# Kernel optimization log

Measured on AMD Instinct MI355X. Metric: run time of the kernel, lower is better.

## Reference

```python
import jax, jax.numpy as jnp
import numpy as np

N = 50000      # nodes
E = 800000     # edges
IN = 128       # in_channels
HID = 64       # hidden_channels (out per head)
H = 4          # heads
ED = 64        # edge_dim
HC = H * HID   # concat output width


def segment_softmax(logits, seg, num_segments):
    # logits: [E, H], softmax over edges sharing the same destination node
    m = jax.ops.segment_max(logits, seg, num_segments=num_segments)
    m = jnp.where(jnp.isfinite(m), m, 0.0)
    e = jnp.exp(logits - m[seg])
    s = jax.ops.segment_sum(e, seg, num_segments=num_segments)
    return e / (s[seg] + 1e-16)


def gatv2_layer(x, src, dst, edge_attr, Wl, bl, Wr, br, We, att, bias):
    # GATv2Conv (PyG, concat=True, negative_slope=0.2), dropout off (eval)
    Hh, C = att.shape
    xl = (x @ Wl + bl).reshape(-1, Hh, C)   # [N,H,C] source transform
    xr = (x @ Wr + br).reshape(-1, Hh, C)   # [N,H,C] target transform
    ee = (edge_attr @ We).reshape(-1, Hh, C)  # [E,H,C]
    m = jax.nn.leaky_relu(xl[src] + xr[dst] + ee, 0.2)  # [E,H,C]
    logits = jnp.einsum('ehc,hc->eh', m, att)           # [E,H]
    alpha = segment_softmax(logits, dst, x.shape[0])    # [E,H]
    out = jax.ops.segment_sum(alpha[:, :, None] * xl[src], dst,
                              num_segments=x.shape[0])  # [N,H,C]
    return out.reshape(x.shape[0], Hh * C) + bias


def setup_inputs() -> dict:
    key = jax.random.key(0)
    ks = jax.random.split(key, 20)
    g = lambda k, shape, s=0.05: (jax.random.normal(k, shape, jnp.float32) * s)
    inp = {
        'x': jax.random.normal(ks[0], (N, IN), jnp.float32),
        'edge_index': jax.random.randint(ks[1], (2, E), 0, N, dtype=jnp.int32),
        'edge_attr': jax.random.normal(ks[2], (E, ED), jnp.float32),
        # layer 1: in_channels -> heads*hidden
        'Wl1': g(ks[3], (IN, HC)), 'bl1': jnp.zeros((HC,), jnp.float32),
        'Wr1': g(ks[4], (IN, HC)), 'br1': jnp.zeros((HC,), jnp.float32),
        'We1': g(ks[5], (ED, HC)),
        'att1': g(ks[6], (H, HID)), 'bias1': jnp.zeros((HC,), jnp.float32),
        # layer 2: heads*hidden -> heads*hidden
        'Wl2': g(ks[7], (HC, HC)), 'bl2': jnp.zeros((HC,), jnp.float32),
        'Wr2': g(ks[8], (HC, HC)), 'br2': jnp.zeros((HC,), jnp.float32),
        'We2': g(ks[9], (ED, HC)),
        'att2': g(ks[10], (H, HID)), 'bias2': jnp.zeros((HC,), jnp.float32),
    }
    return inp


def reference(x, edge_index, edge_attr,
              Wl1, bl1, Wr1, br1, We1, att1, bias1,
              Wl2, bl2, Wr2, br2, We2, att2, bias2):
    src, dst = edge_index[0], edge_index[1]
    h1 = gatv2_layer(x, src, dst, edge_attr, Wl1, bl1, Wr1, br1, We1, att1, bias1)
    h2 = gatv2_layer(h1, src, dst, edge_attr, Wl2, bl2, Wr2, br2, We2, att2, bias2)
    return h2
```

## Files before the change

kernel.cpp:

```cpp
#include <hip/hip_runtime.h>
#include <math.h>

#define NN 50000
#define NE 800000

#define LRELU(v) fmaxf((v), 0.2f * (v))

typedef __attribute__((ext_vector_type(4))) float f32x4;
typedef __attribute__((ext_vector_type(8))) short bf16x8;

static __device__ __forceinline__ unsigned short f2bf(float f) {
  union { float f; unsigned int i; } c; c.f = f;
  unsigned int r = c.i + 0x7fff + ((c.i >> 16) & 1);
  return (unsigned short)(r >> 16);
}
static __device__ __forceinline__ float bflo(unsigned int u) {
  union { unsigned int i; float f; } c; c.i = u << 16; return c.f;
}
static __device__ __forceinline__ float bfhi(unsigned int u) {
  union { unsigned int i; float f; } c; c.i = u & 0xffff0000u; return c.f;
}

__global__ __launch_bounds__(256)
void conv_all(const float* __restrict__ We1, unsigned short* __restrict__ wef1,
              const float* __restrict__ We2, unsigned short* __restrict__ wef2,
              const float* __restrict__ Wl1, unsigned short* __restrict__ wlf1,
              const float* __restrict__ Wr1, unsigned short* __restrict__ wrf1,
              const float* __restrict__ Wl2, unsigned short* __restrict__ wlf2,
              const float* __restrict__ Wr2, unsigned short* __restrict__ wrf2) {
  const int y = blockIdx.y;
  const int g = blockIdx.x * 256 + threadIdx.x;
  if (y < 2) {
    if (g >= 16384) return;
    const float* We = y ? We2 : We1;
    unsigned short* wef = y ? wef2 : wef1;
    const int j = g & 7;
    const int l = (g >> 3) & 63;
    const int t = g >> 9;
    const int n = t & 15, half = t >> 4;
    const int k = half * 32 + (l >> 4) * 8 + j;
    const int c = ((l & 15) >> 2) * 64 + n * 4 + (l & 3);
    wef[g] = f2bf(We[(size_t)k * 256 + c]);
  } else {
    const int K = (y < 4) ? 128 : 256;
    if (g >= K * 256) return;
    const float* W = (y == 2) ? Wl1 : (y == 3) ? Wr1 : (y == 4) ? Wl2 : Wr2;
    unsigned short* wf = (y == 2) ? wlf1 : (y == 3) ? wrf1
                       : (y == 4) ? wlf2 : wrf2;
    const int j = g & 7;
    const int l = (g >> 3) & 63;
    const int fn = g >> 9;
    const int n = fn & 15, ks = fn >> 4;
    const int k = ks * 32 + (l >> 4) * 8 + j;
    const int c = n * 16 + (l & 15);
    wf[g] = f2bf(W[(size_t)k * 256 + c]);
  }
}

template <int KS, int BF>
__global__ __launch_bounds__(256)
void gemm_mfma4(const void* __restrict__ Av,
                const unsigned short* __restrict__ wf0,
                const float* __restrict__ b0, unsigned short* __restrict__ out0,
                const unsigned short* __restrict__ wf1,
                const float* __restrict__ b1, unsigned short* __restrict__ out1) {
  const int mat = blockIdx.y & 1;
  const int nh  = blockIdx.y >> 1;
  const unsigned short* wf = mat ? wf1 : wf0;
  const float* bias        = mat ? b1 : b0;
  unsigned short* outb     = mat ? out1 : out0;

  const int tid = threadIdx.x;
  const int w = tid >> 6, l = tid & 63;
  const int lid = l & 15, lg = l >> 4;
  const int row  = blockIdx.x * 64 + w * 16 + lid;
  const bool rowok = row < NN;
  const int rowv = rowok ? row : NN - 1;
  const int K = KS * 32;

  bf16x8 bfr[KS];
  if (BF) {
    const unsigned short* A = (const unsigned short*)Av;
    const unsigned short* ap = A + (size_t)rowv * K + lg * 8;
#pragma unroll
    for (int ks = 0; ks < KS; ++ks)
      bfr[ks] = *(const bf16x8*)(ap + ks * 32);
  } else {
    const float* A = (const float*)Av;
    const float* ap = A + (size_t)rowv * K + lg * 8;
#pragma unroll
    for (int ks = 0; ks < KS; ++ks) {
      const float4 v0 = *(const float4*)(ap + ks * 32);
      const float4 v1 = *(const float4*)(ap + ks * 32 + 4);
      bf16x8 b;
      b[0]=f2bf(v0.x); b[1]=f2bf(v0.y); b[2]=f2bf(v0.z); b[3]=f2bf(v0.w);
      b[4]=f2bf(v1.x); b[5]=f2bf(v1.y); b[6]=f2bf(v1.z); b[7]=f2bf(v1.w);
      bfr[ks] = b;
    }
  }

  f32x4 acc[8];
#pragma unroll
  for (int n8 = 0; n8 < 8; ++n8) acc[n8] = (f32x4){0.f, 0.f, 0.f, 0.f};

#pragma unroll
  for (int ks = 0; ks < KS; ++ks)
#pragma unroll
    for (int n8 = 0; n8 < 8; ++n8) {
      const int n = nh * 8 + n8;
      const bf16x8 a = *(const bf16x8*)(wf + ((size_t)(ks * 16 + n) * 64 + l) * 8);
      acc[n8] = __builtin_amdgcn_mfma_f32_16x16x32_bf16(a, bfr[ks], acc[n8], 0, 0, 0);
    }

  if (rowok) {
#pragma unroll
    for (int n8 = 0; n8 < 8; ++n8) {
      const int c0 = (nh * 8 + n8) * 16 + lg * 4;
      const float4 bv = *(const float4*)(bias + c0);
      ushort4 o;
      o.x = f2bf(acc[n8][0] + bv.x); o.y = f2bf(acc[n8][1] + bv.y);
      o.z = f2bf(acc[n8][2] + bv.z); o.w = f2bf(acc[n8][3] + bv.w);
      *(ushort4*)(outb + (size_t)row * 256 + c0) = o;
    }
  }
}

__global__ __launch_bounds__(256)
void dst_hist(const int* __restrict__ dst, int* __restrict__ cnt) {
  const int e = blockIdx.x * 256 + threadIdx.x;
  if (e < NE) atomicAdd(&cnt[dst[e]], 1);
}

__global__ __launch_bounds__(1024)
void scan_bsum(const int* __restrict__ cnt, int* __restrict__ bsum, int n) {
  __shared__ int wsum[16];
  const int tid = threadIdx.x;
  const int lane = tid & 63, wid = tid >> 6;
  const int i = blockIdx.x * 1024 + tid;
  int v = (i < n) ? cnt[i] : 0;
#pragma unroll
  for (int off = 32; off >= 1; off >>= 1) v += __shfl_xor(v, off);
  if (lane == 0) wsum[wid] = v;
  __syncthreads();
  if (tid == 0) {
    int s = 0;
#pragma unroll
    for (int k = 0; k < 16; ++k) s += wsum[k];
    bsum[blockIdx.x] = s;
  }
}

__global__ __launch_bounds__(64)
void scan_bsum_scan(int* __restrict__ bsum, int* __restrict__ row_start,
                    int nb, int n) {
  const int lane = threadIdx.x;
  const int v = (lane < nb) ? bsum[lane] : 0;
  int incl = v;
#pragma unroll
  for (int off = 1; off < 64; off <<= 1) {
    const int t = __shfl_up(incl, off);
    if (lane >= off) incl += t;
  }
  if (lane < nb) bsum[lane] = incl - v;
  if (lane == 63) row_start[n] = incl;
}

__global__ __launch_bounds__(1024)
void scan_apply(int* __restrict__ cnt, const int* __restrict__ bsum,
                int* __restrict__ row_start, int n) {
  __shared__ int wsum[16];
  __shared__ int woff[16];
  const int tid = threadIdx.x;
  const int lane = tid & 63, wid = tid >> 6;
  const int i = blockIdx.x * 1024 + tid;
  const int v = (i < n) ? cnt[i] : 0;
  int incl = v;
#pragma unroll
  for (int off = 1; off < 64; off <<= 1) {
    const int t = __shfl_up(incl, off);
    if (lane >= off) incl += t;
  }
  if (lane == 63) wsum[wid] = incl;
  __syncthreads();
  if (wid == 0) {
    const int s = (lane < 16) ? wsum[lane] : 0;
    int si = s;
#pragma unroll
    for (int off = 1; off < 16; off <<= 1) {
      const int t = __shfl_up(si, off);
      if (lane >= off) si += t;
    }
    if (lane < 16) woff[lane] = si - s;
  }
  __syncthreads();
  if (i < n) {
    const int excl = bsum[blockIdx.x] + woff[wid] + incl - v;
    row_start[i] = excl;
    cnt[i] = excl;
  }
}

__global__ __launch_bounds__(256)
void bucket_fill(const int* __restrict__ src, const int* __restrict__ dst,
                 int* __restrict__ cur, int* __restrict__ eid,
                 int* __restrict__ ssrc, int* __restrict__ sdst) {
  const int e = blockIdx.x * 256 + threadIdx.x;
  if (e < NE) {
    const int d = dst[e];
    const int p = atomicAdd(&cur[d], 1);
    eid[p] = e;
    ssrc[p] = src[e];
    sdst[p] = d;
  }
}

__global__ __launch_bounds__(256)
void conv_eab(const float* __restrict__ ea, const int* __restrict__ eid,
              unsigned short* __restrict__ eab) {
  const int g = blockIdx.x * 256 + threadIdx.x;
  const int p = g >> 4, c4 = (g & 15) * 4;
  const int e = eid[p];
  const float4 v = *(const float4*)(ea + (size_t)e * 64 + c4);
  ushort4 o;
  o.x = f2bf(v.x); o.y = f2bf(v.y); o.z = f2bf(v.z); o.w = f2bf(v.w);
  *(ushort4*)(eab + (size_t)p * 64 + c4) = o;
}

static __device__ __forceinline__ float edge_epilogue(
    const unsigned short* __restrict__ xlp,
    const unsigned short* __restrict__ xrp,
    const float* __restrict__ attp,
    const unsigned short* __restrict__ wef,
    bf16x8 f0, bf16x8 f1, int l) {
  float ph = 0.f;
#pragma unroll
  for (int nn = 0; nn < 8; ++nn) {
    const bf16x8 w00 = *(const bf16x8*)(wef + ((size_t)(0  + 2 * nn)     * 64 + l) * 8);
    const bf16x8 w01 = *(const bf16x8*)(wef + ((size_t)(16 + 2 * nn)     * 64 + l) * 8);
    const bf16x8 w10 = *(const bf16x8*)(wef + ((size_t)(0  + 2 * nn + 1) * 64 + l) * 8);
    const bf16x8 w11 = *(const bf16x8*)(wef + ((size_t)(16 + 2 * nn + 1) * 64 + l) * 8);

    f32x4 a0 = (f32x4){0.f,0.f,0.f,0.f}, a1 = (f32x4){0.f,0.f,0.f,0.f};
    a0 = __builtin_amdgcn_mfma_f32_16x16x32_bf16(w00, f0, a0, 0, 0, 0);
    a0 = __builtin_amdgcn_mfma_f32_16x16x32_bf16(w01, f1, a0, 0, 0, 0);
    a1 = __builtin_amdgcn_mfma_f32_16x16x32_bf16(w10, f0, a1, 0, 0, 0);
    a1 = __builtin_amdgcn_mfma_f32_16x16x32_bf16(w11, f1, a1, 0, 0, 0);

    const int c0 = nn * 8;
    const uint4 xu = *(const uint4*)(xlp + c0);
    const uint4 ru = *(const uint4*)(xrp + c0);
    const float4 at0 = *(const float4*)(attp + c0);
    const float4 at1 = *(const float4*)(attp + c0 + 4);
    float v;
    v = a0[0] + bflo(xu.x) + bflo(ru.x); v = LRELU(v); ph += v * at0.x;
    v = a0[1] + bfhi(xu.x) + bfhi(ru.x); v = LRELU(v); ph += v * at0.y;
    v = a0[2] + bflo(xu.y) + bflo(ru.y); v = LRELU(v); ph += v * at0.z;
    v = a0[3] + bfhi(xu.y) + bfhi(ru.y); v = LRELU(v); ph += v * at0.w;
    v = a1[0] + bflo(xu.z) + bflo(ru.z); v = LRELU(v); ph += v * at1.x;
    v = a1[1] + bfhi(xu.z) + bfhi(ru.z); v = LRELU(v); ph += v * at1.y;
    v = a1[2] + bflo(xu.w) + bflo(ru.w); v = LRELU(v); ph += v * at1.z;
    v = a1[3] + bfhi(xu.w) + bfhi(ru.w); v = LRELU(v); ph += v * at1.w;
  }
  return ph;
}

template <int EAB>
__global__ __launch_bounds__(128)
void edge_logits_swap(const float* __restrict__ ea,
                      const unsigned short* __restrict__ eab,
                      const unsigned short* __restrict__ wef,
                      const unsigned short* __restrict__ xlb,
                      const unsigned short* __restrict__ xrb,
                      const float* __restrict__ att,
                      const int* __restrict__ eid,
                      const int* __restrict__ ssrc, const int* __restrict__ sdst,
                      float* __restrict__ elog) {
  __shared__ unsigned short sxl[2][16 * 264];

  const int tid = threadIdx.x;
  const int w = tid >> 6, l = tid & 63;
  const int lid = l & 15, lg = l >> 4;
  const int base = (blockIdx.x * 2 + w) * 32;
  const int pA = base + lid;
  const int pB = base + 16 + lid;

  unsigned short* myxl = sxl[w];
  const int srow_r = l >> 5;
  const int unit   = l & 31;

  bf16x8 fA0, fA1;
  if (EAB) {
    fA0 = *(const bf16x8*)(eab + (size_t)pA * 64 + lg * 8);
    fA1 = *(const bf16x8*)(eab + (size_t)pA * 64 + 32 + lg * 8);
  } else {
    const int e = eid[pA];
    const float* ap = ea + (size_t)e * 64 + lg * 8;
    const float4 v00 = *(const float4*)(ap);
    const float4 v01 = *(const float4*)(ap + 4);
    const float4 v10 = *(const float4*)(ap + 32);
    const float4 v11 = *(const float4*)(ap + 36);
    fA0[0]=f2bf(v00.x); fA0[1]=f2bf(v00.y); fA0[2]=f2bf(v00.z); fA0[3]=f2bf(v00.w);
    fA0[4]=f2bf(v01.x); fA0[5]=f2bf(v01.y); fA0[6]=f2bf(v01.z); fA0[7]=f2bf(v01.w);
    fA1[0]=f2bf(v10.x); fA1[1]=f2bf(v10.y); fA1[2]=f2bf(v10.z); fA1[3]=f2bf(v10.w);
    fA1[4]=f2bf(v11.x); fA1[5]=f2bf(v11.y); fA1[6]=f2bf(v11.z); fA1[7]=f2bf(v11.w);
  }
  const int dA = sdst[pA];

  uint4 gA[8];
#pragma unroll
  for (int i = 0; i < 8; ++i) {
    const int row = i * 2 + srow_r;
    const int srow = ssrc[base + row];
    gA[i] = *(const uint4*)(xlb + (size_t)srow * 256 + unit * 8);
  }

  bf16x8 fB0, fB1;
  if (EAB) {
    fB0 = *(const bf16x8*)(eab + (size_t)pB * 64 + lg * 8);
    fB1 = *(const bf16x8*)(eab + (size_t)pB * 64 + 32 + lg * 8);
  } else {
    const int e = eid[pB];
    const float* ap = ea + (size_t)e * 64 + lg * 8;
    const float4 v00 = *(const float4*)(ap);
    const float4 v01 = *(const float4*)(ap + 4);
    const float4 v10 = *(const float4*)(ap + 32);
    const float4 v11 = *(const float4*)(ap + 36);
    fB0[0]=f2bf(v00.x); fB0[1]=f2bf(v00.y); fB0[2]=f2bf(v00.z); fB0[3]=f2bf(v00.w);
    fB0[4]=f2bf(v01.x); fB0[5]=f2bf(v01.y); fB0[6]=f2bf(v01.z); fB0[7]=f2bf(v01.w);
    fB1[0]=f2bf(v10.x); fB1[1]=f2bf(v10.y); fB1[2]=f2bf(v10.z); fB1[3]=f2bf(v10.w);
    fB1[4]=f2bf(v11.x); fB1[5]=f2bf(v11.y); fB1[6]=f2bf(v11.z); fB1[7]=f2bf(v11.w);
  }
  const int dB = sdst[pB];

  uint4 gB[8];
#pragma unroll
  for (int i = 0; i < 8; ++i) {
    const int row = i * 2 + srow_r;
    const int srow = ssrc[base + 16 + row];
    gB[i] = *(const uint4*)(xlb + (size_t)srow * 256 + unit * 8);
  }

#pragma unroll
  for (int i = 0; i < 8; ++i) {
    const int row = i * 2 + srow_r;
    *(uint4*)&myxl[row * 264 + unit * 8] = gA[i];
  }
  const float phA = edge_epilogue(myxl + lid * 264 + lg * 64,
                                  xrb + (size_t)dA * 256 + lg * 64,
                                  att + lg * 64, wef, fA0, fA1, l);
  elog[(size_t)pA * 4 + lg] = expf(phA);

#pragma unroll
  for (int i = 0; i < 8; ++i) {
    const int row = i * 2 + srow_r;
    *(uint4*)&myxl[row * 264 + unit * 8] = gB[i];
  }
  const float phB = edge_epilogue(myxl + lid * 264 + lg * 64,
                                  xrb + (size_t)dB * 256 + lg * 64,
                                  att + lg * 64, wef, fB0, fB1, l);
  elog[(size_t)pB * 4 + lg] = expf(phB);
}

template <int FINAL>
__global__ __launch_bounds__(256)
void aggregate(const unsigned short* __restrict__ xlb,
               const float* __restrict__ elog,
               const int* __restrict__ ssrc, const int* __restrict__ row_start,
               const float* __restrict__ bias, float* __restrict__ outf,
               unsigned short* __restrict__ outb) {
  const int wid  = threadIdx.x >> 6;
  const int lane = threadIdx.x & 63;
  const int d    = blockIdx.x * 4 + wid;
  const int h = lane >> 4;
  const int c = lane * 4;
  float ax = 0.f, ay = 0.f, az = 0.f, aw = 0.f;
  float dtot = 0.f;
  const int beg = row_start[d], end = row_start[d + 1];
  int p = beg;
  for (; p + 4 <= end; p += 4) {
    const float e0 = elog[(size_t)(p + 0) * 4 + h];
    const float e1 = elog[(size_t)(p + 1) * 4 + h];
    const float e2 = elog[(size_t)(p + 2) * 4 + h];
    const float e3 = elog[(size_t)(p + 3) * 4 + h];
    const int s0 = ssrc[p + 0], s1 = ssrc[p + 1];
    const int s2 = ssrc[p + 2], s3 = ssrc[p + 3];
    const uint2 x0 = *(const uint2*)(xlb + (size_t)s0 * 256 + c);
    const uint2 x1 = *(const uint2*)(xlb + (size_t)s1 * 256 + c);
    const uint2 x2 = *(const uint2*)(xlb + (size_t)s2 * 256 + c);
    const uint2 x3 = *(const uint2*)(xlb + (size_t)s3 * 256 + c);
    ax += e0*bflo(x0.x) + e1*bflo(x1.x) + e2*bflo(x2.x) + e3*bflo(x3.x);
    ay += e0*bfhi(x0.x) + e1*bfhi(x1.x) + e2*bfhi(x2.x) + e3*bfhi(x3.x);
    az += e0*bflo(x0.y) + e1*bflo(x1.y) + e2*bflo(x2.y) + e3*bflo(x3.y);
    aw += e0*bfhi(x0.y) + e1*bfhi(x1.y) + e2*bfhi(x2.y) + e3*bfhi(x3.y);
    dtot += e0 + e1 + e2 + e3;
  }
  for (; p < end; ++p) {
    const float ev = elog[(size_t)p * 4 + h];
    const int s = ssrc[p];
    const uint2 xv = *(const uint2*)(xlb + (size_t)s * 256 + c);
    ax += ev * bflo(xv.x); ay += ev * bfhi(xv.x);
    az += ev * bflo(xv.y); aw += ev * bfhi(xv.y);
    dtot += ev;
  }
  const float inv = 1.f / (dtot + 1e-16f);
  const float4 bv = *(const float4*)(bias + c);
  float4 o;
  o.x = bv.x + ax * inv; o.y = bv.y + ay * inv;
  o.z = bv.z + az * inv; o.w = bv.w + aw * inv;
  if (FINAL) {
    *(float4*)(outf + (size_t)d * 256 + c) = o;
  } else {
    ushort4 ob;
    ob.x = f2bf(o.x); ob.y = f2bf(o.y); ob.z = f2bf(o.z); ob.w = f2bf(o.w);
    *(ushort4*)(outb + (size_t)d * 256 + c) = ob;
  }
}

extern "C" void kernel_launch(void* const* d_in, const int* in_sizes, int n_in,
                              void* d_out, int out_size, void* d_ws, size_t ws_size,
                              hipStream_t stream) {
  const float* x    = (const float*)d_in[0];
  const int*   ei   = (const int*)d_in[1];
  const float* ea   = (const float*)d_in[2];
  const float* Wl1  = (const float*)d_in[3];
  const float* bl1  = (const float*)d_in[4];
  const float* Wr1  = (const float*)d_in[5];
  const float* br1  = (const float*)d_in[6];
  const float* We1  = (const float*)d_in[7];
  const float* att1 = (const float*)d_in[8];
  const float* bias1= (const float*)d_in[9];
  const float* Wl2  = (const float*)d_in[10];
  const float* bl2  = (const float*)d_in[11];
  const float* Wr2  = (const float*)d_in[12];
  const float* br2  = (const float*)d_in[13];
  const float* We2  = (const float*)d_in[14];
  const float* att2 = (const float*)d_in[15];
  const float* bias2= (const float*)d_in[16];

  float* out = (float*)d_out;
  float* ws  = (float*)d_ws;

  float* elog = ws;
  unsigned short* xlb  = (unsigned short*)(elog + (size_t)NE * 4);
  unsigned short* xrb  = xlb + (size_t)NN * 256;
  unsigned short* h1b  = xrb + (size_t)NN * 256;
  unsigned short* wef1 = h1b + (size_t)NN * 256;
  unsigned short* wef2 = wef1 + 16384;
  unsigned short* wlf1 = wef2 + 16384;
  unsigned short* wrf1 = wlf1 + 32768;
  unsigned short* wlf2 = wrf1 + 32768;
  unsigned short* wrf2 = wlf2 + 65536;
  int* cur       = (int*)(wrf2 + 65536);
  int* row_start = cur + NN;
  int* bsum      = row_start + NN + 1;
  int* eid       = bsum + 64;
  int* ssrc      = eid + NE;
  int* sdst      = ssrc + NE;
  unsigned short* eab = (unsigned short*)(sdst + NE);
  const size_t need_eab =
      ((char*)(eab + (size_t)NE * 64)) - (char*)d_ws;
  const bool use_eab = ws_size >= need_eab;

  const int* src = ei;
  const int* dst = ei + NE;

  const int ggrid = (NN + 63) / 64;
  const int egrid = NE / 64;
  const int epb   = (NE + 255) / 256;
  const int agrid = NN / 4;
  const int nb    = (NN + 1023) / 1024;

  hipMemsetAsync(cur, 0, NN * sizeof(int), stream);
  conv_all<<<dim3(256, 6), 256, 0, stream>>>(We1, wef1, We2, wef2,
                                             Wl1, wlf1, Wr1, wrf1,
                                             Wl2, wlf2, Wr2, wrf2);
  dst_hist<<<epb, 256, 0, stream>>>(dst, cur);
  scan_bsum<<<nb, 1024, 0, stream>>>(cur, bsum, NN);
  scan_bsum_scan<<<1, 64, 0, stream>>>(bsum, row_start, nb, NN);
  scan_apply<<<nb, 1024, 0, stream>>>(cur, bsum, row_start, NN);
  bucket_fill<<<epb, 256, 0, stream>>>(src, dst, cur, eid, ssrc, sdst);
  if (use_eab)
    conv_eab<<<NE * 16 / 256, 256, 0, stream>>>(ea, eid, eab);

  gemm_mfma4<4, 0><<<dim3(ggrid, 4), 256, 0, stream>>>(x, wlf1, bl1, xlb,
                                                       wrf1, br1, xrb);
  if (use_eab)
    edge_logits_swap<1><<<egrid, 128, 0, stream>>>(ea, eab, wef1, xlb, xrb,
                                                   att1, eid, ssrc, sdst, elog);
  else
    edge_logits_swap<0><<<egrid, 128, 0, stream>>>(ea, eab, wef1, xlb, xrb,
                                                   att1, eid, ssrc, sdst, elog);
  aggregate<0><<<agrid, 256, 0, stream>>>(xlb, elog, ssrc, row_start, bias1,
                                          nullptr, h1b);

  gemm_mfma4<8, 1><<<dim3(ggrid, 4), 256, 0, stream>>>(h1b, wlf2, bl2, xlb,
                                                       wrf2, br2, xrb);
  if (use_eab)
    edge_logits_swap<1><<<egrid, 128, 0, stream>>>(ea, eab, wef2, xlb, xrb,
                                                   att2, eid, ssrc, sdst, elog);
  else
    edge_logits_swap<0><<<egrid, 128, 0, stream>>>(ea, eab, wef2, xlb, xrb,
                                                   att2, eid, ssrc, sdst, elog);
  aggregate<1><<<agrid, 256, 0, stream>>>(xlb, elog, ssrc, row_start, bias2,
                                          out, nullptr);
}
```

Measured before the change: 604.0 us.

## Gather source features directly into LDS with swizzled layout in edge-logit kernel

Replaces the register-staged gather of source node features with global_load_lds direct-to-LDS transfers, using an XOR swizzle instead of row padding to avoid bank conflicts. Each wave now handles 16 edges instead of 32, and the grid is doubled to match. Source indices are broadcast with shuffles instead of reloaded per lane. The aim is to cut VGPR pressure and the copy through registers. The cost is less memory-level parallelism per wave and a full vmcnt(0) wait before compute.

```diff
diff --git a/kernel.cpp b/kernel.cpp
--- a/kernel.cpp
+++ b/kernel.cpp
@@ -226,12 +226,66 @@
   *(ushort4*)(eab + (size_t)p * 64 + c4) = o;
 }
 
-static __device__ __forceinline__ float edge_epilogue(
-    const unsigned short* __restrict__ xlp,
-    const unsigned short* __restrict__ xrp,
-    const float* __restrict__ attp,
-    const unsigned short* __restrict__ wef,
-    bf16x8 f0, bf16x8 f1, int l) {
+template <int EAB>
+__global__ __launch_bounds__(128)
+void edge_logits_glds(const float* __restrict__ ea,
+                      const unsigned short* __restrict__ eab,
+                      const unsigned short* __restrict__ wef,
+                      const unsigned short* __restrict__ xlb,
+                      const unsigned short* __restrict__ xrb,
+                      const float* __restrict__ att,
+                      const int* __restrict__ eid,
+                      const int* __restrict__ ssrc, const int* __restrict__ sdst,
+                      float* __restrict__ elog) {
+  __shared__ unsigned short sxl[2][16 * 256];
+
+  const int tid = threadIdx.x;
+  const int w = tid >> 6, l = tid & 63;
+  const int lid = l & 15, lg = l >> 4;
+  const int base = (blockIdx.x * 2 + w) * 16;
+  const int p = base + lid;
+
+  const int my_s = ssrc[p];
+
+  const int rr = l >> 5;
+  const int u_phys = l & 31;
+#pragma unroll
+  for (int i = 0; i < 8; ++i) {
+    const int r = 2 * i + rr;
+    const int srow = __shfl(my_s, r);
+    const int u = u_phys ^ (r & 7);
+    const unsigned short* gsrc = xlb + (size_t)srow * 256 + u * 8;
+    __builtin_amdgcn_global_load_lds(
+        (const __attribute__((address_space(1))) unsigned int*)gsrc,
+        (__attribute__((address_space(3))) unsigned int*)&sxl[w][i * 512],
+        16, 0, 0);
+  }
+
+  bf16x8 f0, f1;
+  if (EAB) {
+    f0 = *(const bf16x8*)(eab + (size_t)p * 64 + lg * 8);
+    f1 = *(const bf16x8*)(eab + (size_t)p * 64 + 32 + lg * 8);
+  } else {
+    const int e = eid[p];
+    const float* ap = ea + (size_t)e * 64 + lg * 8;
+    const float4 v00 = *(const float4*)(ap);
+    const float4 v01 = *(const float4*)(ap + 4);
+    const float4 v10 = *(const float4*)(ap + 32);
+    const float4 v11 = *(const float4*)(ap + 36);
+    f0[0]=f2bf(v00.x); f0[1]=f2bf(v00.y); f0[2]=f2bf(v00.z); f0[3]=f2bf(v00.w);
+    f0[4]=f2bf(v01.x); f0[5]=f2bf(v01.y); f0[6]=f2bf(v01.z); f0[7]=f2bf(v01.w);
+    f1[0]=f2bf(v10.x); f1[1]=f2bf(v10.y); f1[2]=f2bf(v10.z); f1[3]=f2bf(v10.w);
+    f1[4]=f2bf(v11.x); f1[5]=f2bf(v11.y); f1[6]=f2bf(v11.z); f1[7]=f2bf(v11.w);
+  }
+  const int d = sdst[p];
+  const unsigned short* xrp = xrb + (size_t)d * 256 + lg * 64;
+  const float* attp = att + lg * 64;
+  const unsigned short* xlrow = &sxl[w][lid * 256];
+  const int lsw = lid & 7;
+
+  asm volatile("s_waitcnt vmcnt(0)" ::: "memory");
+  __builtin_amdgcn_sched_barrier(0);
+
   float ph = 0.f;
 #pragma unroll
   for (int nn = 0; nn < 8; ++nn) {
@@ -246,11 +300,11 @@
     a1 = __builtin_amdgcn_mfma_f32_16x16x32_bf16(w10, f0, a1, 0, 0, 0);
     a1 = __builtin_amdgcn_mfma_f32_16x16x32_bf16(w11, f1, a1, 0, 0, 0);
 
-    const int c0 = nn * 8;
-    const uint4 xu = *(const uint4*)(xlp + c0);
-    const uint4 ru = *(const uint4*)(xrp + c0);
-    const float4 at0 = *(const float4*)(attp + c0);
-    const float4 at1 = *(const float4*)(attp + c0 + 4);
+    const int up = (lg * 8 + nn) ^ lsw;
+    const uint4 xu = *(const uint4*)(xlrow + up * 8);
+    const uint4 ru = *(const uint4*)(xrp + nn * 8);
+    const float4 at0 = *(const float4*)(attp + nn * 8);
+    const float4 at1 = *(const float4*)(attp + nn * 8 + 4);
     float v;
     v = a0[0] + bflo(xu.x) + bflo(ru.x); v = LRELU(v); ph += v * at0.x;
     v = a0[1] + bfhi(xu.x) + bfhi(ru.x); v = LRELU(v); ph += v * at0.y;
@@ -261,104 +315,8 @@
     v = a1[2] + bflo(xu.w) + bflo(ru.w); v = LRELU(v); ph += v * at1.z;
     v = a1[3] + bfhi(xu.w) + bfhi(ru.w); v = LRELU(v); ph += v * at1.w;
   }
-  return ph;
-}
-
-template <int EAB>
-__global__ __launch_bounds__(128)
-void edge_logits_swap(const float* __restrict__ ea,
-                      const unsigned short* __restrict__ eab,
-                      const unsigned short* __restrict__ wef,
-                      const unsigned short* __restrict__ xlb,
-                      const unsigned short* __restrict__ xrb,
-                      const float* __restrict__ att,
-                      const int* __restrict__ eid,
-                      const int* __restrict__ ssrc, const int* __restrict__ sdst,
-                      float* __restrict__ elog) {
-  __shared__ unsigned short sxl[2][16 * 264];
-
-  const int tid = threadIdx.x;
-  const int w = tid >> 6, l = tid & 63;
-  const int lid = l & 15, lg = l >> 4;
-  const int base = (blockIdx.x * 2 + w) * 32;
-  const int pA = base + lid;
-  const int pB = base + 16 + lid;
-
-  unsigned short* myxl = sxl[w];
-  const int srow_r = l >> 5;
-  const int unit   = l & 31;
-
-  bf16x8 fA0, fA1;
-  if (EAB) {
-    fA0 = *(const bf16x8*)(eab + (size_t)pA * 64 + lg * 8);
-    fA1 = *(const bf16x8*)(eab + (size_t)pA * 64 + 32 + lg * 8);
-  } else {
-    const int e = eid[pA];
-    const float* ap = ea + (size_t)e * 64 + lg * 8;
-    const float4 v00 = *(const float4*)(ap);
-    const float4 v01 = *(const float4*)(ap + 4);
-    const float4 v10 = *(const float4*)(ap + 32);
-    const float4 v11 = *(const float4*)(ap + 36);
-    fA0[0]=f2bf(v00.x); fA0[1]=f2bf(v00.y); fA0[2]=f2bf(v00.z); fA0[3]=f2bf(v00.w);
-    fA0[4]=f2bf(v01.x); fA0[5]=f2bf(v01.y); fA0[6]=f2bf(v01.z); fA0[7]=f2bf(v01.w);
-    fA1[0]=f2bf(v10.x); fA1[1]=f2bf(v10.y); fA1[2]=f2bf(v10.z); fA1[3]=f2bf(v10.w);
-    fA1[4]=f2bf(v11.x); fA1[5]=f2bf(v11.y); fA1[6]=f2bf(v11.z); fA1[7]=f2bf(v11.w);
-  }
-  const int dA = sdst[pA];
-
-  uint4 gA[8];
-#pragma unroll
-  for (int i = 0; i < 8; ++i) {
-    const int row = i * 2 + srow_r;
-    const int srow = ssrc[base + row];
-    gA[i] = *(const uint4*)(xlb + (size_t)srow * 256 + unit * 8);
-  }
-
-  bf16x8 fB0, fB1;
-  if (EAB) {
-    fB0 = *(const bf16x8*)(eab + (size_t)pB * 64 + lg * 8);
-    fB1 = *(const bf16x8*)(eab + (size_t)pB * 64 + 32 + lg * 8);
-  } else {
-    const int e = eid[pB];
-    const float* ap = ea + (size_t)e * 64 + lg * 8;
-    const float4 v00 = *(const float4*)(ap);
-    const float4 v01 = *(const float4*)(ap + 4);
-    const float4 v10 = *(const float4*)(ap + 32);
-    const float4 v11 = *(const float4*)(ap + 36);
-    fB0[0]=f2bf(v00.x); fB0[1]=f2bf(v00.y); fB0[2]=f2bf(v00.z); fB0[3]=f2bf(v00.w);
-    fB0[4]=f2bf(v01.x); fB0[5]=f2bf(v01.y); fB0[6]=f2bf(v01.z); fB0[7]=f2bf(v01.w);
-    fB1[0]=f2bf(v10.x); fB1[1]=f2bf(v10.y); fB1[2]=f2bf(v10.z); fB1[3]=f2bf(v10.w);
-    fB1[4]=f2bf(v11.x); fB1[5]=f2bf(v11.y); fB1[6]=f2bf(v11.z); fB1[7]=f2bf(v11.w);
-  }
-  const int dB = sdst[pB];
-
-  uint4 gB[8];
-#pragma unroll
-  for (int i = 0; i < 8; ++i) {
-    const int row = i * 2 + srow_r;
-    const int srow = ssrc[base + 16 + row];
-    gB[i] = *(const uint4*)(xlb + (size_t)srow * 256 + unit * 8);
-  }
-
-#pragma unroll
-  for (int i = 0; i < 8; ++i) {
-    const int row = i * 2 + srow_r;
-    *(uint4*)&myxl[row * 264 + unit * 8] = gA[i];
-  }
-  const float phA = edge_epilogue(myxl + lid * 264 + lg * 64,
-                                  xrb + (size_t)dA * 256 + lg * 64,
-                                  att + lg * 64, wef, fA0, fA1, l);
-  elog[(size_t)pA * 4 + lg] = expf(phA);
-
-#pragma unroll
-  for (int i = 0; i < 8; ++i) {
-    const int row = i * 2 + srow_r;
-    *(uint4*)&myxl[row * 264 + unit * 8] = gB[i];
-  }
-  const float phB = edge_epilogue(myxl + lid * 264 + lg * 64,
-                                  xrb + (size_t)dB * 256 + lg * 64,
-                                  att + lg * 64, wef, fB0, fB1, l);
-  elog[(size_t)pB * 4 + lg] = expf(phB);
+
+  elog[(size_t)p * 4 + lg] = expf(ph);
 }
 
 template <int FINAL>
@@ -465,7 +423,7 @@
   const int* dst = ei + NE;
 
   const int ggrid = (NN + 63) / 64;
-  const int egrid = NE / 64;
+  const int egrid = NE / 32;
   const int epb   = (NE + 255) / 256;
   const int agrid = NN / 4;
   const int nb    = (NN + 1023) / 1024;
@@ -485,10 +443,10 @@
   gemm_mfma4<4, 0><<<dim3(ggrid, 4), 256, 0, stream>>>(x, wlf1, bl1, xlb,
                                                        wrf1, br1, xrb);
   if (use_eab)
-    edge_logits_swap<1><<<egrid, 128, 0, stream>>>(ea, eab, wef1, xlb, xrb,
+    edge_logits_glds<1><<<egrid, 128, 0, stream>>>(ea, eab, wef1, xlb, xrb,
                                                    att1, eid, ssrc, sdst, elog);
   else
-    edge_logits_swap<0><<<egrid, 128, 0, stream>>>(ea, eab, wef1, xlb, xrb,
+    edge_logits_glds<0><<<egrid, 128, 0, stream>>>(ea, eab, wef1, xlb, xrb,
                                                    att1, eid, ssrc, sdst, elog);
   aggregate<0><<<agrid, 256, 0, stream>>>(xlb, elog, ssrc, row_start, bias1,
                                           nullptr, h1b);
@@ -496,10 +454,10 @@
   gemm_mfma4<8, 1><<<dim3(ggrid, 4), 256, 0, stream>>>(h1b, wlf2, bl2, xlb,
                                                        wrf2, br2, xrb);
   if (use_eab)
-    edge_logits_swap<1><<<egrid, 128, 0, stream>>>(ea, eab, wef2, xlb, xrb,
+    edge_logits_glds<1><<<egrid, 128, 0, stream>>>(ea, eab, wef2, xlb, xrb,
                                                    att2, eid, ssrc, sdst, elog);
   else
-    edge_logits_swap<0><<<egrid, 128, 0, stream>>>(ea, eab, wef2, xlb, xrb,
+    edge_logits_glds<0><<<egrid, 128, 0, stream>>>(ea, eab, wef2, xlb, xrb,
                                                    att2, eid, ssrc, sdst, elog);
   aggregate<1><<<agrid, 256, 0, stream>>>(xlb, elog, ssrc, row_start, bias2,
                                           out, nullptr);
```

Measured after the change: 626.0 us. +3.7%, slower.
